# Performance work log

Measured on AMD Instinct MI355X. Metric: run time of the kernel, lower is better.

Reference implementation:

```python
import jax, jax.numpy as jnp
import numpy as np

N, E = 50000, 800000
IN_D, HID, OUT_D, PROJ = 256, 512, 64, 64


def spmm(src, dst, val, x, n):
    # out[i] = sum_{e: src[e]==i} val[e] * x[dst[e]]  (torch.sparse.mm with COO indices [src;dst])
    return jax.ops.segment_sum(val[:, None] * x[dst], src, num_segments=n)


def sparse_avg(src, dst, val, h, n):
    deg = jnp.maximum(jax.ops.segment_sum(val, src, num_segments=n), 1.0)
    return spmm(src, dst, val, h, n) / deg[:, None]


def gcn(x, W, b, src, dst, val, n):
    # dropout is identity in eval mode; linear -> SpMM -> relu
    return jax.nn.relu(spmm(src, dst, val, x @ W + b, n))


def mlp(x, W1, b1, a, W3, b3):
    h = x @ W1 + b1
    h = jnp.where(h >= 0, h, a[0] * h)  # PReLU, single shared weight
    return h @ W3 + b3


def bilinear(h, c, W, b):
    # nn.Bilinear(proj, proj, 1): h W c^T + b, per node
    return jnp.einsum('nd,de,ne->n', h, W, c) + b[0]


def discriminator(c, h_pl, h_mi, W, b):
    return jnp.stack([bilinear(h_pl, c, W, b), bilinear(h_mi, c, W, b)], axis=1)  # [N,2]


def setup_inputs():
    key = jax.random.key(0)
    ks = iter(jax.random.split(key, 32))
    nk = lambda: next(ks)

    def edges():
        src = jax.random.randint(nk(), (E,), 0, N, dtype=jnp.int32)
        dst = jax.random.randint(nk(), (E,), 0, N, dtype=jnp.int32)
        val = jax.random.uniform(nk(), (E,), dtype=jnp.float32)
        return src, dst, val

    adj_src, adj_dst, adj_val = edges()
    gdc_src, gdc_dst, gdc_val = edges()
    neigh_src, neigh_dst, neigh_val = edges()
    diff_src, diff_dst, diff_val = edges()
    feat = jax.random.normal(nk(), (N, IN_D), dtype=jnp.float32)
    perm = jnp.flip(jnp.arange(N, dtype=jnp.int32))  # fixed deterministic permutation (stands in for randperm)
    p = lambda *s: jax.random.normal(nk(), s, dtype=jnp.float32) * 0.05
    return dict(
        feat=feat,
        adj_src=adj_src, adj_dst=adj_dst, adj_val=adj_val,
        gdc_src=gdc_src, gdc_dst=gdc_dst, gdc_val=gdc_val,
        neigh_src=neigh_src, neigh_dst=neigh_dst, neigh_val=neigh_val,
        diff_src=diff_src, diff_dst=diff_dst, diff_val=diff_val,
        perm=perm,
        W_enc=p(IN_D, OUT_D), b_enc=jnp.zeros((OUT_D,), jnp.float32),
        W_dec=p(OUT_D, IN_D), b_dec=jnp.zeros((IN_D,), jnp.float32),
        W1=p(OUT_D, HID), b1=jnp.zeros((HID,), jnp.float32),
        prelu_a=jnp.full((1,), 0.25, jnp.float32),
        W3=p(HID, PROJ), b3=jnp.zeros((PROJ,), jnp.float32),
        W_disc=p(PROJ, PROJ), b_disc=jnp.zeros((1,), jnp.float32),
    )


def reference(feat, adj_src, adj_dst, adj_val, gdc_src, gdc_dst, gdc_val,
              neigh_src, neigh_dst, neigh_val, diff_src, diff_dst, diff_val,
              perm, W_enc, b_enc, W_dec, b_dec, W1, b1, prelu_a, W3, b3,
              W_disc, b_disc):
    h = gcn(feat, W_enc, b_enc, adj_src, adj_dst, adj_val, N)
    h_g = gcn(feat, W_enc, b_enc, gdc_src, gdc_dst, gdc_val, N)
    shuf_h = gcn(feat[perm], W_enc, b_enc, adj_src, adj_dst, adj_val, N)
    emb = gcn(h, W_dec, b_dec, adj_src, adj_dst, adj_val, N)
    z = mlp(h, W1, b1, prelu_a, W3, b3)
    z_g = mlp(h_g, W1, b1, prelu_a, W3, b3)
    shuf_z = mlp(shuf_h, W1, b1, prelu_a, W3, b3)
    g = mlp(jax.nn.sigmoid(sparse_avg(neigh_src, neigh_dst, neigh_val, h, N)), W1, b1, prelu_a, W3, b3)
    g_g = mlp(jax.nn.sigmoid(sparse_avg(diff_src, diff_dst, diff_val, h_g, N)), W1, b1, prelu_a, W3, b3)
    ret = discriminator(g_g, z, shuf_z, W_disc, b_disc)
    ret_a = discriminator(g, z_g, shuf_z, W_disc, b_disc)
    return (emb, ret, ret_a)
```

## Files before the change

kernel.cpp:

```cpp
#include <hip/hip_runtime.h>
#include <cstdint>

#define IND 256
#define HIDD 512
#define ND 64
#define BK 48
#define BINW 256
#define BCAP 4608
#define ECHUNK 4096

typedef __attribute__((ext_vector_type(8))) short bf8;
typedef __attribute__((ext_vector_type(4))) float f4;

__device__ inline unsigned pack_bf16(float lo, float hi) {
  unsigned a = __float_as_uint(lo);
  unsigned b = __float_as_uint(hi);
  a = a + 0x7fffu + ((a >> 16) & 1u);
  b = b + 0x7fffu + ((b >> 16) & 1u);
  return (a >> 16) | (b & 0xffff0000u);
}
__device__ inline unsigned short cvt_bf16(float f) {
  unsigned u = __float_as_uint(f);
  u = (u + 0x7fffu + ((u >> 16) & 1u)) >> 16;
  return (unsigned short)u;
}

__global__ __launch_bounds__(256) void binpass_kernel(
    const int* __restrict__ s0, const int* __restrict__ s1,
    const int* __restrict__ s2, const int* __restrict__ s3,
    const int* __restrict__ d0, const int* __restrict__ d1,
    const int* __restrict__ d2, const int* __restrict__ d3,
    const float* __restrict__ v0, const float* __restrict__ v1,
    const float* __restrict__ v2, const float* __restrict__ v3,
    int* __restrict__ gcnt, uint2* __restrict__ be, int e, int nbin) {
  int set = blockIdx.y;
  const int* src = (set == 0) ? s0 : (set == 1) ? s1 : (set == 2) ? s2 : s3;
  const int* dst = (set == 0) ? d0 : (set == 1) ? d1 : (set == 2) ? d2 : d3;
  const float* val = (set == 0) ? v0 : (set == 1) ? v1 : (set == 2) ? v2 : v3;
  __shared__ int hist[256];
  __shared__ int basel[256];
  int tid = threadIdx.x;
  for (int i = tid; i < 256; i += 256) hist[i] = 0;
  __syncthreads();
  int e0 = blockIdx.x * ECHUNK;
  int bins[16];
  uint2 recs[16];
#pragma unroll
  for (int k = 0; k < 16; ++k) {
    int i = e0 + tid + k * 256;
    bool valid = i < e;
    int s = 0, d = 0;
    unsigned u = 0;
    if (valid) {
      s = src[i]; d = dst[i];
      u = __float_as_uint(val[i]);
      u = (u + 0x7fffu + ((u >> 16) & 1u)) & 0xFFFF0000u;
    }
    int b = s >> 8;
    bins[k] = valid ? b : -1;
    recs[k].x = u | (unsigned)d;
    recs[k].y = (unsigned)s;
    if (valid) atomicAdd(&hist[b], 1);
  }
  __syncthreads();
  for (int i = tid; i < nbin; i += 256) {
    int c = hist[i];
    basel[i] = c ? atomicAdd(&gcnt[set * nbin + i], c) : 0;
    hist[i] = 0;
  }
  __syncthreads();
#pragma unroll
  for (int k = 0; k < 16; ++k) {
    int b = bins[k];
    if (b >= 0) {
      int loc = atomicAdd(&hist[b], 1);
      int p = basel[b] + loc;
      if (p < BCAP) be[((size_t)set * nbin + b) * BCAP + p] = recs[k];
    }
  }
}

__global__ __launch_bounds__(256) void bucketize_kernel(const int* __restrict__ gcnt,
    const uint2* __restrict__ be, int* __restrict__ pos, unsigned* __restrict__ bk,
    int n, int nbin) {
  int set = blockIdx.y, bin = blockIdx.x;
  int node0 = bin * BINW;
  int nn = min(BINW, n - node0);
  __shared__ unsigned lb[BINW * BK];
  __shared__ int lpos[BINW];
  int tid = threadIdx.x;
  for (int i = tid; i < BINW; i += 256) lpos[i] = 0;
  {
    uint4* l4 = (uint4*)lb;
    const uint4 z = {0u, 0u, 0u, 0u};
    for (int i = tid; i < BINW * BK / 4; i += 256) l4[i] = z;
  }
  __syncthreads();
  int cnt = min(gcnt[set * nbin + bin], BCAP);
  const uint2* src = be + ((size_t)set * nbin + bin) * BCAP;
  for (int i = tid; i < cnt; i += 256) {
    uint2 r = src[i];
    int sl = (int)r.y - node0;
    int slot = atomicAdd(&lpos[sl], 1);
    if (slot < BK) lb[sl * BK + slot] = r.x;
  }
  __syncthreads();
  uint4* dst4 = (uint4*)(bk + ((size_t)set * n + node0) * BK);
  const uint4* src4 = (const uint4*)lb;
  int nq = nn * (BK / 4);
  for (int i = tid; i < nq; i += 256) dst4[i] = src4[i];
  for (int i = tid; i < nn; i += 256) pos[(size_t)set * n + node0 + i] = lpos[i];
}

__global__ __launch_bounds__(256) void spmmA_kernel(const unsigned* __restrict__ bk,
    const int* __restrict__ pos, const unsigned short* __restrict__ x1,
    const unsigned short* __restrict__ x1p,
    unsigned short* __restrict__ hb, unsigned short* __restrict__ shb,
    unsigned short* __restrict__ hgb, float* __restrict__ rsA, int n) {
  int row = (blockIdx.x * 256 + threadIdx.x) >> 6;
  if (row >= n) return;
  row = __builtin_amdgcn_readfirstlane(row);
  int lane = threadIdx.x & 63;
  int set = blockIdx.y;
  const unsigned* bb = bk + ((size_t)set * n + row) * BK;
  int deg = __builtin_amdgcn_readfirstlane(min(pos[(size_t)set * n + row], BK));
  unsigned rc = bb[min(lane, BK - 1)];
  int ne = (deg + 3) & ~3;
  if (set == 0) {
    float acc = 0.f, acc2 = 0.f, sv = 0.f;
    for (int e = 0; e < ne; e += 4) {
#pragma unroll
      for (int k = 0; k < 4; ++k) {
        unsigned r = (unsigned)__builtin_amdgcn_readlane((int)rc, e + k);
        float v = __uint_as_float(r & 0xffff0000u);
        int d = (int)(r & 0xffffu);
        float xv = __uint_as_float((unsigned)x1[((size_t)d << 6) + lane] << 16);
        float yv = __uint_as_float((unsigned)x1p[((size_t)d << 6) + lane] << 16);
        acc = fmaf(v, xv, acc);
        acc2 = fmaf(v, yv, acc2);
        sv += v;
      }
    }
    hb[(size_t)row * 64 + lane] = cvt_bf16(fmaxf(acc, 0.f));
    shb[(size_t)row * 64 + lane] = cvt_bf16(fmaxf(acc2, 0.f));
    if (lane == 0) rsA[row] = sv;
  } else {
    float acc = 0.f;
    for (int e = 0; e < ne; e += 4) {
#pragma unroll
      for (int k = 0; k < 4; ++k) {
        unsigned r = (unsigned)__builtin_amdgcn_readlane((int)rc, e + k);
        float v = __uint_as_float(r & 0xffff0000u);
        int d = (int)(r & 0xffffu);
        float xv = __uint_as_float((unsigned)x1[((size_t)d << 6) + lane] << 16);
        acc = fmaf(v, xv, acc);
      }
    }
    hgb[(size_t)row * 64 + lane] = cvt_bf16(fmaxf(acc, 0.f));
  }
}

__global__ __launch_bounds__(256) void spmmB_kernel(const unsigned* __restrict__ bk,
    const int* __restrict__ pos, const unsigned short* __restrict__ hb,
    const unsigned short* __restrict__ hgb, float* __restrict__ tb,
    unsigned short* __restrict__ s1b, unsigned short* __restrict__ s2b, int n) {
  int row = (blockIdx.x * 256 + threadIdx.x) >> 6;
  if (row >= n) return;
  row = __builtin_amdgcn_readfirstlane(row);
  int lane = threadIdx.x & 63;
  int set = blockIdx.y;
  int bset = (set == 0) ? 0 : (set == 1) ? 2 : 3;
  const unsigned short* x = (set == 2) ? hgb : hb;
  const unsigned* bb = bk + ((size_t)bset * n + row) * BK;
  int deg = __builtin_amdgcn_readfirstlane(min(pos[(size_t)bset * n + row], BK));
  unsigned rc = bb[min(lane, BK - 1)];
  int ne = (deg + 3) & ~3;
  if (set == 0) {
    float acc = 0.f;
    for (int e = 0; e < ne; e += 4) {
#pragma unroll
      for (int k = 0; k < 4; ++k) {
        unsigned r = (unsigned)__builtin_amdgcn_readlane((int)rc, e + k);
        float v = __uint_as_float(r & 0xffff0000u);
        int d = (int)(r & 0xffffu);
        float xv = __uint_as_float((unsigned)x[((size_t)d << 6) + lane] << 16);
        acc = fmaf(v, xv, acc);
      }
    }
    tb[(size_t)row * 64 + lane] = acc;
  } else {
    float acc = 0.f, sv = 0.f;
    for (int e = 0; e < ne; e += 4) {
#pragma unroll
      for (int k = 0; k < 4; ++k) {
        unsigned r = (unsigned)__builtin_amdgcn_readlane((int)rc, e + k);
        float v = __uint_as_float(r & 0xffff0000u);
        int d = (int)(r & 0xffffu);
        float xv = __uint_as_float((unsigned)x[((size_t)d << 6) + lane] << 16);
        acc = fmaf(v, xv, acc);
        sv += v;
      }
    }
    float dg = fmaxf(sv, 1.f);
    float o = 1.f / (1.f + __expf(-acc / dg));
    unsigned short* out = (set == 1) ? s1b : s2b;
    out[(size_t)row * 64 + lane] = cvt_bf16(o);
  }
}

__global__ __launch_bounds__(256) void permx_kernel(const uint4* __restrict__ x1,
    const int* __restrict__ perm, uint4* __restrict__ x1p, int n) {
  int t = blockIdx.x * 256 + threadIdx.x;
  if (t >= n * 8) return;
  int r = t >> 3, j = t & 7;
  int q = perm[r];
  x1p[(size_t)r * 8 + j] = x1[(size_t)q * 8 + j];
}

__global__ __launch_bounds__(256) void gemm_x1_kernel(const float* __restrict__ feat,
    const float* __restrict__ W, const float* __restrict__ b, unsigned short* __restrict__ x1, int n) {
  __shared__ float fl[32][260];
  int tid = threadIdx.x;
  int r0 = blockIdx.x * 32;
#pragma unroll
  for (int it = 0; it < 8; ++it) {
    int idx = tid + it * 256;
    int rr = idx >> 6, cc = (idx & 63) * 4;
    int r = min(r0 + rr, n - 1);
    *(float4*)&fl[rr][cc] = *(const float4*)&feat[(size_t)r * IND + cc];
  }
  __syncthreads();
  int c16 = tid & 15, rg = tid >> 4;
  float4 bq = *(const float4*)&b[c16 * 4];
  float acc[2][4];
#pragma unroll
  for (int t = 0; t < 2; ++t) {
    acc[t][0] = bq.x; acc[t][1] = bq.y; acc[t][2] = bq.z; acc[t][3] = bq.w;
  }
  for (int k4 = 0; k4 < IND / 4; ++k4) {
    float wk[4][4];
#pragma unroll
    for (int kk = 0; kk < 4; ++kk) {
      float4 w = *(const float4*)&W[(size_t)(k4 * 4 + kk) * 64 + c16 * 4];
      wk[kk][0] = w.x; wk[kk][1] = w.y; wk[kk][2] = w.z; wk[kk][3] = w.w;
    }
    float xr[2][4];
#pragma unroll
    for (int t = 0; t < 2; ++t) {
      float4 xv = *(const float4*)&fl[rg * 2 + t][k4 * 4];
      xr[t][0] = xv.x; xr[t][1] = xv.y; xr[t][2] = xv.z; xr[t][3] = xv.w;
    }
#pragma unroll
    for (int kk = 0; kk < 4; ++kk)
#pragma unroll
      for (int t = 0; t < 2; ++t)
#pragma unroll
        for (int q = 0; q < 4; ++q)
          acc[t][q] += xr[t][kk] * wk[kk][q];
  }
#pragma unroll
  for (int t = 0; t < 2; ++t) {
    int r = r0 + rg * 2 + t;
    if (r < n) {
      uint2 o; o.x = pack_bf16(acc[t][0], acc[t][1]); o.y = pack_bf16(acc[t][2], acc[t][3]);
      *(uint2*)&x1[(size_t)r * 64 + c16 * 4] = o;
    }
  }
}

__global__ __launch_bounds__(256) void gemm_emb_kernel(const float* __restrict__ t,
    const float* __restrict__ W, const float* __restrict__ b, const float* __restrict__ rs,
    float* __restrict__ out, int n) {
  __shared__ float tl[16][68];
  int tid = threadIdx.x;
  int r0 = blockIdx.x * 16;
  {
    int rr = tid >> 4, cc = (tid & 15) * 4;
    int r = min(r0 + rr, n - 1);
    *(float4*)&tl[rr][cc] = *(const float4*)&t[(size_t)r * 64 + cc];
  }
  __syncthreads();
  int c64 = tid & 63, rg4 = tid >> 6;
  float4 bq = *(const float4*)&b[c64 * 4];
  float acc[4][4];
#pragma unroll
  for (int tt = 0; tt < 4; ++tt) {
    float rsn = rs[min(r0 + rg4 * 4 + tt, n - 1)];
    acc[tt][0] = rsn * bq.x; acc[tt][1] = rsn * bq.y; acc[tt][2] = rsn * bq.z; acc[tt][3] = rsn * bq.w;
  }
  for (int k4 = 0; k4 < 16; ++k4) {
    float wk[4][4];
#pragma unroll
    for (int kk = 0; kk < 4; ++kk) {
      float4 w = *(const float4*)&W[(size_t)(k4 * 4 + kk) * IND + c64 * 4];
      wk[kk][0] = w.x; wk[kk][1] = w.y; wk[kk][2] = w.z; wk[kk][3] = w.w;
    }
    float xr[4][4];
#pragma unroll
    for (int tt = 0; tt < 4; ++tt) {
      float4 xv = *(const float4*)&tl[rg4 * 4 + tt][k4 * 4];
      xr[tt][0] = xv.x; xr[tt][1] = xv.y; xr[tt][2] = xv.z; xr[tt][3] = xv.w;
    }
#pragma unroll
    for (int kk = 0; kk < 4; ++kk)
#pragma unroll
      for (int tt = 0; tt < 4; ++tt)
#pragma unroll
        for (int q = 0; q < 4; ++q)
          acc[tt][q] += xr[tt][kk] * wk[kk][q];
  }
#pragma unroll
  for (int tt = 0; tt < 4; ++tt) {
    int r = r0 + rg4 * 4 + tt;
    if (r < n) {
      float4 o;
      o.x = fmaxf(acc[tt][0], 0.f); o.y = fmaxf(acc[tt][1], 0.f);
      o.z = fmaxf(acc[tt][2], 0.f); o.w = fmaxf(acc[tt][3], 0.f);
      *(float4*)&out[(size_t)r * IND + c64 * 4] = o;
    }
  }
}

__global__ __launch_bounds__(256) void pack_w_kernel(const float* __restrict__ W,
    short* __restrict__ out, int K, int Ncols) {
  int t = blockIdx.x * 256 + threadIdx.x;
  int KS = K >> 5;
  int total = KS * (Ncols >> 4) * 64;
  if (t >= total) return;
  int l = t & 63;
  int tk = t >> 6;
  int tile = tk / KS, ks = tk - tile * KS;
  int q = l >> 4, i16 = l & 15;
  int col = tile * 16 + i16;
  unsigned pk[4];
#pragma unroll
  for (int jp = 0; jp < 4; ++jp) {
    int k = ks * 32 + q * 8 + jp * 2;
    float f0 = W[(size_t)k * Ncols + col];
    float f1 = W[(size_t)(k + 1) * Ncols + col];
    pk[jp] = pack_bf16(f0, f1);
  }
  uint4 o; o.x = pk[0]; o.y = pk[1]; o.z = pk[2]; o.w = pk[3];
  *(uint4*)&out[(size_t)t * 8] = o;
}

__global__ __launch_bounds__(256) void mlp_mfma_kernel(const unsigned short* __restrict__ in,
    const short* __restrict__ W1f, const float* __restrict__ b1, const float* __restrict__ ap,
    const short* __restrict__ W3f, const float* __restrict__ b3, float* __restrict__ out, int n) {
  __shared__ short il[64 * 72];
  __shared__ short hl[64 * 264];
  int tid = threadIdx.x;
  int w = tid >> 6, l = tid & 63;
  int q = l >> 4, i16 = l & 15;
  int r0 = blockIdx.x * 64;
  float a = ap[0];
#pragma unroll
  for (int it = 0; it < 4; ++it) {
    int idx = tid + it * 256;
    int rr = idx >> 4, cc = (idx & 15) * 4;
    int r = min(r0 + rr, n - 1);
    *(uint2*)&il[rr * 72 + cc] = *(const uint2*)&in[(size_t)r * 64 + cc];
  }
  __syncthreads();
  bf8 bfr[4][2];
#pragma unroll
  for (int rg = 0; rg < 4; ++rg)
#pragma unroll
    for (int ks = 0; ks < 2; ++ks)
      bfr[rg][ks] = *(const bf8*)&il[(rg * 16 + i16) * 72 + ks * 32 + q * 8];

  f4 accz[4];
  {
    float bz = b3[w * 16 + i16];
#pragma unroll
    for (int rg = 0; rg < 4; ++rg) { accz[rg][0] = bz; accz[rg][1] = bz; accz[rg][2] = bz; accz[rg][3] = bz; }
  }

  for (int c = 0; c < 2; ++c) {
    if (c) __syncthreads();
#pragma unroll
    for (int mt4 = 0; mt4 < 4; ++mt4) {
      int mtg = c * 16 + w * 4 + mt4;
      bf8 af0 = *(const bf8*)&W1f[(size_t)((mtg * 2 + 0) * 64 + l) * 8];
      bf8 af1 = *(const bf8*)&W1f[(size_t)((mtg * 2 + 1) * 64 + l) * 8];
      float4 bb = *(const float4*)&b1[mtg * 16 + q * 4];
#pragma unroll
      for (int rg = 0; rg < 4; ++rg) {
        f4 acc; acc[0] = bb.x; acc[1] = bb.y; acc[2] = bb.z; acc[3] = bb.w;
        acc = __builtin_amdgcn_mfma_f32_16x16x32_bf16(af0, bfr[rg][0], acc, 0, 0, 0);
        acc = __builtin_amdgcn_mfma_f32_16x16x32_bf16(af1, bfr[rg][1], acc, 0, 0, 0);
        float h0 = acc[0] >= 0.f ? acc[0] : a * acc[0];
        float h1 = acc[1] >= 0.f ? acc[1] : a * acc[1];
        float h2 = acc[2] >= 0.f ? acc[2] : a * acc[2];
        float h3 = acc[3] >= 0.f ? acc[3] : a * acc[3];
        uint2 p; p.x = pack_bf16(h0, h1); p.y = pack_bf16(h2, h3);
        *(uint2*)&hl[(rg * 16 + i16) * 264 + 64 * w + mt4 * 16 + q * 4] = p;
      }
    }
    __syncthreads();
#pragma unroll
    for (int ksl = 0; ksl < 8; ++ksl) {
      int ksg = c * 8 + ksl;
      bf8 wf = *(const bf8*)&W3f[(size_t)((w * 16 + ksg) * 64 + l) * 8];
#pragma unroll
      for (int rg = 0; rg < 4; ++rg) {
        bf8 hf = *(const bf8*)&hl[(rg * 16 + i16) * 264 + ksl * 32 + q * 8];
        accz[rg] = __builtin_amdgcn_mfma_f32_16x16x32_bf16(hf, wf, accz[rg], 0, 0, 0);
      }
    }
  }
#pragma unroll
  for (int rg = 0; rg < 4; ++rg) {
#pragma unroll
    for (int r = 0; r < 4; ++r) {
      int row = r0 + rg * 16 + q * 4 + r;
      if (row < n) out[(size_t)row * 64 + w * 16 + i16] = accz[rg][r];
    }
  }
}

__global__ __launch_bounds__(256) void disc2_kernel(const float* __restrict__ zb,
    const float* __restrict__ W, const float* __restrict__ bp,
    float* __restrict__ ret, float* __restrict__ ret_a, int n) {
  int y = blockIdx.y;
  const float* hp = y ? (zb + (size_t)n * 64) : zb;
  const float* hm = zb + (size_t)2 * n * 64;
  const float* c = y ? (zb + (size_t)3 * n * 64) : (zb + (size_t)4 * n * 64);
  float* r = y ? ret_a : ret;
  __shared__ float wl[64][65];
  __shared__ float cl[16][64];
  int tid = threadIdx.x;
  for (int i = tid; i < 64 * 64; i += 256) wl[i >> 6][i & 63] = W[i];
  int nb = blockIdx.x * 16;
  for (int i = tid; i < 16 * 64; i += 256) {
    int nn = i >> 6, ee = i & 63;
    cl[nn][ee] = c[(size_t)min(nb + nn, n - 1) * 64 + ee];
  }
  __syncthreads();
  int w = tid >> 6, lane = tid & 63;
  float b = bp[0];
#pragma unroll
  for (int it = 0; it < 4; ++it) {
    int nn = w * 4 + it;
    int node = nb + nn;
    int nd = min(node, n - 1);
    float u = 0.f;
#pragma unroll 8
    for (int e = 0; e < 64; ++e) u += wl[lane][e] * cl[nn][e];
    float r0v = hp[(size_t)nd * 64 + lane] * u;
    float r1v = hm[(size_t)nd * 64 + lane] * u;
#pragma unroll
    for (int o = 32; o > 0; o >>= 1) {
      r0v += __shfl_xor(r0v, o, 64);
      r1v += __shfl_xor(r1v, o, 64);
    }
    if (lane == 0 && node < n) {
      r[(size_t)node * 2] = r0v + b;
      r[(size_t)node * 2 + 1] = r1v + b;
    }
  }
}

extern "C" void kernel_launch(void* const* d_in, const int* in_sizes, int n_in,
                              void* d_out, int out_size, void* d_ws, size_t ws_size,
                              hipStream_t stream) {
  const float* feat = (const float*)d_in[0];
  const int* srcs[4] = {(const int*)d_in[1], (const int*)d_in[4], (const int*)d_in[7], (const int*)d_in[10]};
  const int* dsts[4] = {(const int*)d_in[2], (const int*)d_in[5], (const int*)d_in[8], (const int*)d_in[11]};
  const float* vals[4] = {(const float*)d_in[3], (const float*)d_in[6], (const float*)d_in[9], (const float*)d_in[12]};
  const int* perm = (const int*)d_in[13];
  const float* W_enc = (const float*)d_in[14];
  const float* b_enc = (const float*)d_in[15];
  const float* W_dec = (const float*)d_in[16];
  const float* b_dec = (const float*)d_in[17];
  const float* W1 = (const float*)d_in[18];
  const float* b1 = (const float*)d_in[19];
  const float* pa = (const float*)d_in[20];
  const float* W3 = (const float*)d_in[21];
  const float* b3 = (const float*)d_in[22];
  const float* Wd = (const float*)d_in[23];
  const float* bd = (const float*)d_in[24];
  (void)n_in; (void)ws_size;

  const int N = in_sizes[13];
  const int E = in_sizes[1];
  const int nbin = (N + BINW - 1) / BINW;

  char* ws = (char*)d_ws;
  size_t off = 0;
  auto alloc = [&](size_t bytes) -> void* {
    void* p = ws + off;
    off += (bytes + 255) & ~(size_t)255;
    return p;
  };
  const size_t nodeh = (size_t)N * 64 * 2;
  const size_t nodef = (size_t)N * 64 * 4;
  unsigned short* x1b = (unsigned short*)alloc(nodeh);
  unsigned short* hseq = (unsigned short*)alloc(5 * nodeh);
  unsigned short* hb  = hseq;
  unsigned short* hgb = hseq + (size_t)N * 64;
  unsigned short* shb = hseq + (size_t)2 * N * 64;
  unsigned short* s1b = hseq + (size_t)3 * N * 64;
  unsigned short* s2b = hseq + (size_t)4 * N * 64;
  float* tb = (float*)alloc(nodef);
  float* zb = (float*)alloc(5 * nodef);
  int*      pos = (int*)alloc((size_t)4 * N * 4);
  unsigned* bkt = (unsigned*)alloc((size_t)4 * N * BK * 4);
  int*      gcnt = (int*)alloc((size_t)4 * nbin * 4);
  uint2*    be = (uint2*)alloc((size_t)4 * nbin * BCAP * 8);
  float*    rsA = (float*)alloc((size_t)N * 4);
  short* W1f  = (short*)alloc((size_t)ND * HIDD * 2);
  short* W3f  = (short*)alloc((size_t)HIDD * ND * 2);
  unsigned short* x1p = (unsigned short*)be;

  hipMemsetAsync(gcnt, 0, (size_t)4 * nbin * 4, stream);

  pack_w_kernel<<<16, 256, 0, stream>>>(W1, W1f, ND, HIDD);
  pack_w_kernel<<<16, 256, 0, stream>>>(W3, W3f, HIDD, ND);

  int eb1 = (E + ECHUNK - 1) / ECHUNK;
  binpass_kernel<<<dim3(eb1, 4), 256, 0, stream>>>(
      srcs[0], srcs[1], srcs[2], srcs[3],
      dsts[0], dsts[1], dsts[2], dsts[3],
      vals[0], vals[1], vals[2], vals[3], gcnt, be, E, nbin);
  bucketize_kernel<<<dim3(nbin, 4), 256, 0, stream>>>(gcnt, be, pos, bkt, N, nbin);

  gemm_x1_kernel<<<(N + 31) / 32, 256, 0, stream>>>(feat, W_enc, b_enc, x1b, N);
  permx_kernel<<<(N * 8 + 255) / 256, 256, 0, stream>>>((const uint4*)x1b, perm, (uint4*)x1p, N);

  int nb4 = (N + 3) / 4;
  spmmA_kernel<<<dim3(nb4, 2), 256, 0, stream>>>(bkt, pos, x1b, x1p, hb, shb, hgb, rsA, N);
  spmmB_kernel<<<dim3(nb4, 3), 256, 0, stream>>>(bkt, pos, hb, hgb, tb, s1b, s2b, N);

  float* out = (float*)d_out;
  gemm_emb_kernel<<<(N + 15) / 16, 256, 0, stream>>>(tb, W_dec, b_dec, rsA, out, N);

  mlp_mfma_kernel<<<(5 * N + 63) / 64, 256, 0, stream>>>(hseq, W1f, b1, pa, W3f, b3, zb, 5 * N);

  float* ret = out + (size_t)N * 256;
  float* ret_a = ret + (size_t)N * 2;
  disc2_kernel<<<dim3((N + 15) / 16, 2), 256, 0, stream>>>(zb, Wd, bd, ret, ret_a, N);
}
```

Measured before the change: 510.6 us.

## Retile encoder and decoder GEMMs with shared-memory 4x4 register blocking

Rewrites the two FP32 GEMM kernels (feat@W_enc and t@W_dec) as classic 64-row tiles with transposed activations and weights staged in shared memory. Each thread now computes a 4x4 output block. In the encoder, K is streamed in chunks of 32. The decoder GEMM gains a second grid dimension over output column blocks. This is meant to raise FMA-per-load reuse and cut the per-iteration global weight reads of the old kernels. The cost is more shared memory and synchronisation per block, plus transposed LDS writes that may cause bank conflicts.

Result: slower. 1.030 ms (+101.7%).

```diff
diff --git a/kernel.cpp b/kernel.cpp
--- a/kernel.cpp
+++ b/kernel.cpp
@@ -219,51 +219,50 @@
 
 __global__ __launch_bounds__(256) void gemm_x1_kernel(const float* __restrict__ feat,
     const float* __restrict__ W, const float* __restrict__ b, unsigned short* __restrict__ x1, int n) {
-  __shared__ float fl[32][260];
+  __shared__ float ft[32][68];
+  __shared__ float wc[32][64];
   int tid = threadIdx.x;
-  int r0 = blockIdx.x * 32;
-#pragma unroll
-  for (int it = 0; it < 8; ++it) {
-    int idx = tid + it * 256;
-    int rr = idx >> 6, cc = (idx & 63) * 4;
-    int r = min(r0 + rr, n - 1);
-    *(float4*)&fl[rr][cc] = *(const float4*)&feat[(size_t)r * IND + cc];
-  }
-  __syncthreads();
-  int c16 = tid & 15, rg = tid >> 4;
-  float4 bq = *(const float4*)&b[c16 * 4];
-  float acc[2][4];
-#pragma unroll
-  for (int t = 0; t < 2; ++t) {
-    acc[t][0] = bq.x; acc[t][1] = bq.y; acc[t][2] = bq.z; acc[t][3] = bq.w;
-  }
-  for (int k4 = 0; k4 < IND / 4; ++k4) {
-    float wk[4][4];
-#pragma unroll
-    for (int kk = 0; kk < 4; ++kk) {
-      float4 w = *(const float4*)&W[(size_t)(k4 * 4 + kk) * 64 + c16 * 4];
-      wk[kk][0] = w.x; wk[kk][1] = w.y; wk[kk][2] = w.z; wk[kk][3] = w.w;
-    }
-    float xr[2][4];
-#pragma unroll
-    for (int t = 0; t < 2; ++t) {
-      float4 xv = *(const float4*)&fl[rg * 2 + t][k4 * 4];
-      xr[t][0] = xv.x; xr[t][1] = xv.y; xr[t][2] = xv.z; xr[t][3] = xv.w;
-    }
-#pragma unroll
-    for (int kk = 0; kk < 4; ++kk)
-#pragma unroll
-      for (int t = 0; t < 2; ++t)
-#pragma unroll
-        for (int q = 0; q < 4; ++q)
-          acc[t][q] += xr[t][kk] * wk[kk][q];
-  }
-#pragma unroll
-  for (int t = 0; t < 2; ++t) {
-    int r = r0 + rg * 2 + t;
+  int r0 = blockIdx.x * 64;
+  int tx = tid & 15, ty = tid >> 4;
+  float4 bq = *(const float4*)&b[tx * 4];
+  float acc[4][4];
+#pragma unroll
+  for (int i = 0; i < 4; ++i) { acc[i][0] = bq.x; acc[i][1] = bq.y; acc[i][2] = bq.z; acc[i][3] = bq.w; }
+  for (int k0 = 0; k0 < IND; k0 += 32) {
+    if (k0) __syncthreads();
+#pragma unroll
+    for (int it = 0; it < 2; ++it) {
+      int idx = tid + it * 256;
+      int rr = idx >> 3, c4 = (idx & 7) * 4;
+      int r = min(r0 + rr, n - 1);
+      float4 f = *(const float4*)&feat[(size_t)r * IND + k0 + c4];
+      ft[c4 + 0][rr] = f.x; ft[c4 + 1][rr] = f.y; ft[c4 + 2][rr] = f.z; ft[c4 + 3][rr] = f.w;
+    }
+    {
+      int kk = tid >> 4, c4 = (tid & 15) * 4;
+      *(float4*)&wc[kk][c4] = *(const float4*)&W[(size_t)(k0 + kk) * 64 + c4];
+      *(float4*)&wc[kk + 16][c4] = *(const float4*)&W[(size_t)(k0 + kk + 16) * 64 + c4];
+    }
+    __syncthreads();
+#pragma unroll
+    for (int kk = 0; kk < 32; ++kk) {
+      float4 fv = *(const float4*)&ft[kk][ty * 4];
+      float4 wv = *(const float4*)&wc[kk][tx * 4];
+      float fr[4] = {fv.x, fv.y, fv.z, fv.w};
+      float wr[4] = {wv.x, wv.y, wv.z, wv.w};
+#pragma unroll
+      for (int i = 0; i < 4; ++i)
+#pragma unroll
+        for (int j = 0; j < 4; ++j)
+          acc[i][j] = fmaf(fr[i], wr[j], acc[i][j]);
+    }
+  }
+#pragma unroll
+  for (int i = 0; i < 4; ++i) {
+    int r = r0 + ty * 4 + i;
     if (r < n) {
-      uint2 o; o.x = pack_bf16(acc[t][0], acc[t][1]); o.y = pack_bf16(acc[t][2], acc[t][3]);
-      *(uint2*)&x1[(size_t)r * 64 + c16 * 4] = o;
+      uint2 o; o.x = pack_bf16(acc[i][0], acc[i][1]); o.y = pack_bf16(acc[i][2], acc[i][3]);
+      *(uint2*)&x1[(size_t)r * 64 + tx * 4] = o;
     }
   }
 }
@@ -271,52 +270,54 @@
 __global__ __launch_bounds__(256) void gemm_emb_kernel(const float* __restrict__ t,
     const float* __restrict__ W, const float* __restrict__ b, const float* __restrict__ rs,
     float* __restrict__ out, int n) {
-  __shared__ float tl[16][68];
+  __shared__ float tt[64][68];
+  __shared__ float wc[64][64];
   int tid = threadIdx.x;
-  int r0 = blockIdx.x * 16;
-  {
-    int rr = tid >> 4, cc = (tid & 15) * 4;
+  int r0 = blockIdx.x * 64;
+  int c0 = blockIdx.y * 64;
+#pragma unroll
+  for (int it = 0; it < 4; ++it) {
+    int idx = tid + it * 256;
+    int rr = idx >> 4, c4 = (idx & 15) * 4;
     int r = min(r0 + rr, n - 1);
-    *(float4*)&tl[rr][cc] = *(const float4*)&t[(size_t)r * 64 + cc];
-  }
-  __syncthreads();
-  int c64 = tid & 63, rg4 = tid >> 6;
-  float4 bq = *(const float4*)&b[c64 * 4];
+    float4 f = *(const float4*)&t[(size_t)r * 64 + c4];
+    tt[c4 + 0][rr] = f.x; tt[c4 + 1][rr] = f.y; tt[c4 + 2][rr] = f.z; tt[c4 + 3][rr] = f.w;
+  }
+#pragma unroll
+  for (int it = 0; it < 4; ++it) {
+    int idx = tid + it * 256;
+    int kk = idx >> 4, c4 = (idx & 15) * 4;
+    *(float4*)&wc[kk][c4] = *(const float4*)&W[(size_t)kk * IND + c0 + c4];
+  }
+  int tx = tid & 15, ty = tid >> 4;
+  float4 bq = *(const float4*)&b[c0 + tx * 4];
   float acc[4][4];
 #pragma unroll
-  for (int tt = 0; tt < 4; ++tt) {
-    float rsn = rs[min(r0 + rg4 * 4 + tt, n - 1)];
-    acc[tt][0] = rsn * bq.x; acc[tt][1] = rsn * bq.y; acc[tt][2] = rsn * bq.z; acc[tt][3] = rsn * bq.w;
-  }
-  for (int k4 = 0; k4 < 16; ++k4) {
-    float wk[4][4];
-#pragma unroll
-    for (int kk = 0; kk < 4; ++kk) {
-      float4 w = *(const float4*)&W[(size_t)(k4 * 4 + kk) * IND + c64 * 4];
-      wk[kk][0] = w.x; wk[kk][1] = w.y; wk[kk][2] = w.z; wk[kk][3] = w.w;
-    }
-    float xr[4][4];
-#pragma unroll
-    for (int tt = 0; tt < 4; ++tt) {
-      float4 xv = *(const float4*)&tl[rg4 * 4 + tt][k4 * 4];
-      xr[tt][0] = xv.x; xr[tt][1] = xv.y; xr[tt][2] = xv.z; xr[tt][3] = xv.w;
-    }
-#pragma unroll
-    for (int kk = 0; kk < 4; ++kk)
-#pragma unroll
-      for (int tt = 0; tt < 4; ++tt)
-#pragma unroll
-        for (int q = 0; q < 4; ++q)
-          acc[tt][q] += xr[tt][kk] * wk[kk][q];
-  }
-#pragma unroll
-  for (int tt = 0; tt < 4; ++tt) {
-    int r = r0 + rg4 * 4 + tt;
+  for (int i = 0; i < 4; ++i) {
+    float rsn = rs[min(r0 + ty * 4 + i, n - 1)];
+    acc[i][0] = rsn * bq.x; acc[i][1] = rsn * bq.y; acc[i][2] = rsn * bq.z; acc[i][3] = rsn * bq.w;
+  }
+  __syncthreads();
+#pragma unroll
+  for (int kk = 0; kk < 64; ++kk) {
+    float4 fv = *(const float4*)&tt[kk][ty * 4];
+    float4 wv = *(const float4*)&wc[kk][tx * 4];
+    float fr[4] = {fv.x, fv.y, fv.z, fv.w};
+    float wr[4] = {wv.x, wv.y, wv.z, wv.w};
+#pragma unroll
+    for (int i = 0; i < 4; ++i)
+#pragma unroll
+      for (int j = 0; j < 4; ++j)
+        acc[i][j] = fmaf(fr[i], wr[j], acc[i][j]);
+  }
+#pragma unroll
+  for (int i = 0; i < 4; ++i) {
+    int r = r0 + ty * 4 + i;
     if (r < n) {
       float4 o;
-      o.x = fmaxf(acc[tt][0], 0.f); o.y = fmaxf(acc[tt][1], 0.f);
-      o.z = fmaxf(acc[tt][2], 0.f); o.w = fmaxf(acc[tt][3], 0.f);
-      *(float4*)&out[(size_t)r * IND + c64 * 4] = o;
+      o.x = fmaxf(acc[i][0], 0.f); o.y = fmaxf(acc[i][1], 0.f);
+      o.z = fmaxf(acc[i][2], 0.f); o.w = fmaxf(acc[i][3], 0.f);
+      *(float4*)&out[(size_t)r * IND + c0 + tx * 4] = o;
     }
   }
 }
@@ -525,7 +526,7 @@
       vals[0], vals[1], vals[2], vals[3], gcnt, be, E, nbin);
   bucketize_kernel<<<dim3(nbin, 4), 256, 0, stream>>>(gcnt, be, pos, bkt, N, nbin);
 
-  gemm_x1_kernel<<<(N + 31) / 32, 256, 0, stream>>>(feat, W_enc, b_enc, x1b, N);
+  gemm_x1_kernel<<<(N + 63) / 64, 256, 0, stream>>>(feat, W_enc, b_enc, x1b, N);
   permx_kernel<<<(N * 8 + 255) / 256, 256, 0, stream>>>((const uint4*)x1b, perm, (uint4*)x1p, N);
 
   int nb4 = (N + 3) / 4;
@@ -533,7 +534,7 @@
   spmmB_kernel<<<dim3(nb4, 3), 256, 0, stream>>>(bkt, pos, hb, hgb, tb, s1b, s2b, N);
 
   float* out = (float*)d_out;
-  gemm_emb_kernel<<<(N + 15) / 16, 256, 0, stream>>>(tb, W_dec, b_dec, rsA, out, N);
+  gemm_emb_kernel<<<dim3((N + 63) / 64, 4), 256, 0, stream>>>(tb, W_dec, b_dec, rsA, out, N);
 
   mlp_mfma_kernel<<<(5 * N + 63) / 64, 256, 0, stream>>>(hseq, W1f, b1, pa, W3f, b3, zb, 5 * N);
 
```
